# Kernel optimization log

Hardware: AMD Instinct MI355X
Metric: run time of the kernel (lower is better)

The kernel has to match this reference:

```python
import jax, jax.numpy as jnp
import numpy as np

N, C, T, F = 32, 64, 256, 64  # batch, EEG channels, time samples, freq bands


def setup_inputs() -> dict:
    key = jax.random.key(0)
    X = jax.random.normal(key, (N, C, T, F), dtype=jnp.float32)
    gammad = jnp.zeros((), dtype=jnp.float32)  # learned scalar, init 'zeros'
    return {"X": X, "gammad": gammad}


def reference(X, gammad):
    # X: (N, C, T, F) -> (N, F, C, T)
    Xp = jnp.transpose(X, (0, 3, 1, 2))
    # squared norms per channel: (N, F, C, 1)
    R = jnp.sum(Xp * Xp, axis=-1, keepdims=True)
    # Gram matrix over time axis: (N, F, C, C)
    G = jnp.einsum('nfct,nfkt->nfck', Xp, Xp)
    # pairwise squared Euclidean distances between channels
    D = R - 2.0 * G + jnp.swapaxes(R, -1, -2)
    # strictly-upper-triangular entries (excludes diagonal), per (n, f)
    iu, ju = jnp.triu_indices(D.shape[-1], k=1)
    triu = jnp.sqrt(D[..., iu, ju])  # (N, F, C*(C-1)/2)
    # median bandwidth (tfp.stats.percentile q=50 uses 'nearest' interpolation)
    sigma = jnp.quantile(triu, 0.5, axis=-1, method='nearest')  # (N, F)
    denom = 2.0 * jnp.power(10.0, gammad) * jnp.square(sigma)   # (N, F)
    A = jnp.exp(-D / denom[..., None, None])  # (N, F, C, C) RBF affinity
    return A
```

## Files before the change

kernel.cpp:

```cpp
#include <hip/hip_runtime.h>
#include <stdint.h>

typedef _Float16 f16x8 __attribute__((ext_vector_type(8)));
typedef float f32x4 __attribute__((ext_vector_type(4)));

__device__ __forceinline__ uint32_t pack2(float a, float b) {
    union { _Float16 h[2]; uint32_t u; } p;
    p.h[0] = (_Float16)a; p.h[1] = (_Float16)b;
    return p.u;
}

__device__ __forceinline__ uint16_t key16(float v) {
    _Float16 hx = (_Float16)fmaxf(v, 0.0f);
    return __builtin_bit_cast(uint16_t, hx);
}

__device__ __forceinline__ f32x4 MF(f16x8 a, f16x8 b, f32x4 c) {
    return __builtin_amdgcn_mfma_f32_16x16x32_f16(a, b, c, 0, 0, 0);
}

__global__ __launch_bounds__(512, 2)
void gfc_main(const float* __restrict__ X, const float* __restrict__ gp,
              float* __restrict__ out) {
    __shared__ __align__(16) unsigned char XS[65536];
    __shared__ float Rbuf[4][64];

    int j = blockIdx.x;
    int xcd = j & 7, s = j >> 3;
    int gi = s >> 2, fq4 = s & 3;
    int g = gi * 8 + xcd;
    int n = g >> 2, f16g = g & 3;
    int f0 = f16g * 16 + fq4 * 4;

    int tid = threadIdx.x;
    int wid = tid >> 6, lane = tid & 63;
    int w4 = wid & 3, hi = wid >> 2;
    int l4 = lane & 15, lg = lane >> 4;

    float p10 = exp2f(gp[0] * 3.3219280948873623f);
    const float* Xn = X + (size_t)n * 1048576 + f0;

    f32x4 dd[2][4];
    #pragma unroll
    for (int a = 0; a < 2; ++a)
        #pragma unroll
        for (int b = 0; b < 4; ++b) dd[a][b] = f32x4{0, 0, 0, 0};

    float4 pv[8][2];

    auto load_chunk = [&](int t0) {
        #pragma unroll
        for (int k = 0; k < 8; ++k) {
            int c = k * 8 + wid;
            const float* p = Xn + (size_t)c * 16384 + t0 * 64 + lane * 128;
            pv[k][0] = *(const float4*)p;
            pv[k][1] = *(const float4*)(p + 64);
        }
    };
    auto write_chunk = [&]() {
        #pragma unroll
        for (int k = 0; k < 8; ++k) {
            int c = k * 8 + wid;
            int o = c * 256 + ((lane * 4) ^ ((c & 7) << 4));
            *(uint32_t*)(XS + o)         = pack2(pv[k][0].x, pv[k][1].x);
            *(uint32_t*)(XS + 16384 + o) = pack2(pv[k][0].y, pv[k][1].y);
            *(uint32_t*)(XS + 32768 + o) = pack2(pv[k][0].z, pv[k][1].z);
            *(uint32_t*)(XS + 49152 + o) = pack2(pv[k][0].w, pv[k][1].w);
        }
    };
    auto gram_buf = [&]() {
        const unsigned char* bp = XS + w4 * 16384;
        #pragma unroll
        for (int ks = 0; ks < 4; ++ks) {
            f16x8 fr[4];
            #pragma unroll
            for (int i2 = 0; i2 < 4; ++i2)
                fr[i2] = *(const f16x8*)(bp + (i2 * 16 + l4) * 256 +
                                         ((ks * 64 + lg * 16) ^ ((l4 & 7) << 4)));
            if (!hi) {
                #pragma unroll
                for (int tj = 0; tj < 4; ++tj) {
                    dd[0][tj] = MF(fr[tj], fr[0], dd[0][tj]);
                    dd[1][tj] = MF(fr[tj], fr[1], dd[1][tj]);
                }
            } else {
                #pragma unroll
                for (int tj = 0; tj < 4; ++tj) {
                    dd[0][tj] = MF(fr[tj], fr[2], dd[0][tj]);
                    dd[1][tj] = MF(fr[tj], fr[3], dd[1][tj]);
                }
            }
        }
    };

    load_chunk(0);
    write_chunk();
    load_chunk(128);
    __syncthreads();

    gram_buf();
    __syncthreads();

    write_chunk();
    __syncthreads();

    gram_buf();

    {
        f32x4 dg0 = hi ? dd[0][2] : dd[0][0];
        f32x4 dg1 = hi ? dd[1][3] : dd[1][1];
        if (lg == (l4 >> 2)) {
            int r = l4 & 3;
            float v0 = r == 0 ? dg0[0] : r == 1 ? dg0[1] : r == 2 ? dg0[2] : dg0[3];
            float v1 = r == 0 ? dg1[0] : r == 1 ? dg1[1] : r == 2 ? dg1[2] : dg1[3];
            Rbuf[w4][(hi * 2) * 16 + l4] = v0;
            Rbuf[w4][(hi * 2 + 1) * 16 + l4] = v1;
        }
    }
    __syncthreads();

    float Rr0 = Rbuf[w4][(hi * 2) * 16 + l4];
    float Rr1 = Rbuf[w4][(hi * 2 + 1) * 16 + l4];
    #pragma unroll
    for (int tj = 0; tj < 4; ++tj) {
        f32x4 Rc = *(const f32x4*)&Rbuf[w4][tj * 16 + lg * 4];
        #pragma unroll
        for (int r = 0; r < 4; ++r) {
            dd[0][tj][r] = Rr0 + Rc[r] - 2.0f * dd[0][tj][r];
            dd[1][tj][r] = Rr1 + Rc[r] - 2.0f * dd[1][tj][r];
        }
    }

    uint32_t pk[32];
    #pragma unroll
    for (int tt = 0; tt < 2; ++tt) {
        int row = (hi * 2 + tt) * 16 + l4;
        #pragma unroll
        for (int tj = 0; tj < 4; ++tj)
            #pragma unroll
            for (int rp = 0; rp < 2; ++rp) {
                int col0 = tj * 16 + lg * 4 + 2 * rp;
                uint32_t k0 = (row < col0)     ? key16(dd[tt][tj][2 * rp])     : 0x7FFFu;
                uint32_t k1 = (row < col0 + 1) ? key16(dd[tt][tj][2 * rp + 1]) : 0x7FFFu;
                pk[tt * 8 + tj * 2 + rp] = k0 | (k1 << 16);
            }
    }

    {
        uint32_t* base = (uint32_t*)(XS + w4 * 16384);
        uint32_t* mywr = base + hi * 1024;
        #pragma unroll
        for (int e = 0; e < 16; ++e) mywr[e * 64 + lane] = pk[e];
        __syncthreads();
        const uint32_t* prd = base + (hi ^ 1) * 1024;
        #pragma unroll
        for (int e = 0; e < 16; ++e) pk[16 + e] = prd[e * 64 + lane];
    }

    int u = 0;
    for (int bit = 14; bit >= 0; --bit) {
        uint32_t cand = (uint32_t)(u | (1 << bit));
        int cnt = 0;
        #pragma unroll
        for (int i = 0; i < 32; ++i) {
            cnt += ((pk[i] & 0xFFFFu) < cand) ? 1 : 0;
            cnt += ((pk[i] >> 16) < cand) ? 1 : 0;
        }
        #pragma unroll
        for (int off = 32; off; off >>= 1) cnt += __shfl_xor(cnt, off, 64);
        if (cnt <= 1008) u |= (1 << bit);
    }
    float sigma2 = (float)__builtin_bit_cast(_Float16, (uint16_t)u);
    float ninv = -1.0f / (2.0f * p10 * sigma2);

    float* op = out + ((size_t)(n * 64 + f0 + w4) << 12);
    #pragma unroll
    for (int tt = 0; tt < 2; ++tt) {
        int row = (hi * 2 + tt) * 16 + l4;
        #pragma unroll
        for (int tj = 0; tj < 4; ++tj) {
            float4 rv;
            rv.x = __expf(dd[tt][tj][0] * ninv);
            rv.y = __expf(dd[tt][tj][1] * ninv);
            rv.z = __expf(dd[tt][tj][2] * ninv);
            rv.w = __expf(dd[tt][tj][3] * ninv);
            *(float4*)(op + row * 64 + tj * 16 + lg * 4) = rv;
        }
    }
}

extern "C" void kernel_launch(void* const* d_in, const int* in_sizes, int n_in,
                              void* d_out, int out_size, void* d_ws, size_t ws_size,
                              hipStream_t stream) {
    (void)in_sizes; (void)n_in; (void)out_size; (void)d_ws; (void)ws_size;
    const float* X  = (const float*)d_in[0];
    const float* gp = (const float*)d_in[1];
    float* out = (float*)d_out;
    gfc_main<<<512, 512, 0, stream>>>(X, gp, out);
}
```

Baseline: 78.32 us.

## Add fp16 transpose prepass into workspace and read it directly in Gram kernel

A new prep kernel reads X with coalesced loads, converts it to fp16 and transposes it through shared memory into a workspace laid out as (n, f, c, t). The main kernel then loads MFMA fragments straight from that workspace, with no LDS staging and no strided fp32 gathers. This targets the poorly coalesced 16-byte strided reads of the original single kernel. The cost is a second launch plus an extra 64 MB write and read through the workspace. The old kernel is kept as a fallback when the workspace is too small.

```diff
diff --git a/kernel.cpp b/kernel.cpp
--- a/kernel.cpp
+++ b/kernel.cpp
@@ -4,10 +4,13 @@
 typedef _Float16 f16x8 __attribute__((ext_vector_type(8)));
 typedef float f32x4 __attribute__((ext_vector_type(4)));
 
-__device__ __forceinline__ uint32_t pack2(float a, float b) {
-    union { _Float16 h[2]; uint32_t u; } p;
-    p.h[0] = (_Float16)a; p.h[1] = (_Float16)b;
-    return p.u;
+__device__ __forceinline__ f32x4 MF(f16x8 a, f16x8 b, f32x4 c) {
+    return __builtin_amdgcn_mfma_f32_16x16x32_f16(a, b, c, 0, 0, 0);
+}
+
+__device__ __forceinline__ uint16_t h16(float v) {
+    _Float16 h = (_Float16)v;
+    return __builtin_bit_cast(uint16_t, h);
 }
 
 __device__ __forceinline__ uint16_t key16(float v) {
@@ -15,39 +18,206 @@
     return __builtin_bit_cast(uint16_t, hx);
 }
 
-__device__ __forceinline__ f32x4 MF(f16x8 a, f16x8 b, f32x4 c) {
-    return __builtin_amdgcn_mfma_f32_16x16x32_f16(a, b, c, 0, 0, 0);
+__device__ __forceinline__ uint32_t pack2(float a, float b) {
+    return (uint32_t)h16(a) | ((uint32_t)h16(b) << 16);
+}
+
+__global__ __launch_bounds__(256)
+void gfc_prep(const float* __restrict__ X, uint16_t* __restrict__ W) {
+    __shared__ uint16_t T[256 * 66];
+    int n = blockIdx.x >> 6, c = blockIdx.x & 63;
+    int tid = threadIdx.x;
+    const float* src = X + ((size_t)n * 64 + c) * 16384;
+
+    #pragma unroll
+    for (int rb = 0; rb < 2; ++rb) {
+        float4 v[8];
+        #pragma unroll
+        for (int i = 0; i < 8; ++i) {
+            int o = (rb * 8 + i) * 256 + tid;
+            v[i] = *(const float4*)(src + (size_t)o * 4);
+        }
+        #pragma unroll
+        for (int i = 0; i < 8; ++i) {
+            int o = (rb * 8 + i) * 256 + tid;
+            int t = o >> 4, fj = o & 15;
+            uint16_t* row = &T[t * 66 + fj * 4];
+            row[0] = h16(v[i].x);
+            row[1] = h16(v[i].y);
+            row[2] = h16(v[i].z);
+            row[3] = h16(v[i].w);
+        }
+    }
+    __syncthreads();
+
+    int f = tid >> 2, q = tid & 3;
+    uint16_t* dst = W + (((size_t)n * 64 + f) * 64 + c) * 256 + q * 64;
+    #pragma unroll
+    for (int jj = 0; jj < 8; ++jj) {
+        uint32_t w[4];
+        #pragma unroll
+        for (int p = 0; p < 4; ++p) {
+            int t = q * 64 + jj * 8 + p * 2;
+            uint32_t lo = T[t * 66 + f];
+            uint32_t hi = T[(t + 1) * 66 + f];
+            w[p] = lo | (hi << 16);
+        }
+        *(uint4*)(dst + jj * 8) = *(uint4*)w;
+    }
 }
 
 __global__ __launch_bounds__(512, 2)
-void gfc_main(const float* __restrict__ X, const float* __restrict__ gp,
-              float* __restrict__ out) {
+void gfc_main2(const uint16_t* __restrict__ W, const float* __restrict__ gp,
+               float* __restrict__ out) {
+    __shared__ float Rbuf[4][64];
+    __shared__ uint32_t EX[8][1024];
+
+    int j = blockIdx.x;
+    int xcd = j & 7, r = j >> 3;
+    int fq = r & 15, nh = r >> 4;
+    int n = xcd * 4 + nh;
+    int f0 = fq * 4;
+
+    int tid = threadIdx.x;
+    int wid = tid >> 6, lane = tid & 63;
+    int w4 = wid & 3, hi = wid >> 2;
+    int l4 = lane & 15, lg = lane >> 4;
+
+    float p10 = exp2f(gp[0] * 3.3219280948873623f);
+    const uint16_t* Wf = W + ((size_t)n * 64 + f0 + w4) * 16384;
+
+    f32x4 dd[2][4];
+    #pragma unroll
+    for (int a = 0; a < 2; ++a)
+        #pragma unroll
+        for (int b = 0; b < 4; ++b) dd[a][b] = f32x4{0, 0, 0, 0};
+
+    #pragma unroll
+    for (int ks = 0; ks < 8; ++ks) {
+        f16x8 fr[4];
+        #pragma unroll
+        for (int i2 = 0; i2 < 4; ++i2)
+            fr[i2] = *(const f16x8*)(Wf + (i2 * 16 + l4) * 256 + ks * 32 + lg * 8);
+        if (!hi) {
+            #pragma unroll
+            for (int tj = 0; tj < 4; ++tj) {
+                dd[0][tj] = MF(fr[tj], fr[0], dd[0][tj]);
+                dd[1][tj] = MF(fr[tj], fr[1], dd[1][tj]);
+            }
+        } else {
+            #pragma unroll
+            for (int tj = 0; tj < 4; ++tj) {
+                dd[0][tj] = MF(fr[tj], fr[2], dd[0][tj]);
+                dd[1][tj] = MF(fr[tj], fr[3], dd[1][tj]);
+            }
+        }
+    }
+
+    {
+        f32x4 dg0 = hi ? dd[0][2] : dd[0][0];
+        f32x4 dg1 = hi ? dd[1][3] : dd[1][1];
+        if (lg == (l4 >> 2)) {
+            int rr = l4 & 3;
+            float v0 = rr == 0 ? dg0[0] : rr == 1 ? dg0[1] : rr == 2 ? dg0[2] : dg0[3];
+            float v1 = rr == 0 ? dg1[0] : rr == 1 ? dg1[1] : rr == 2 ? dg1[2] : dg1[3];
+            Rbuf[w4][(hi * 2) * 16 + l4] = v0;
+            Rbuf[w4][(hi * 2 + 1) * 16 + l4] = v1;
+        }
+    }
+    __syncthreads();
+
+    float Rr0 = Rbuf[w4][(hi * 2) * 16 + l4];
+    float Rr1 = Rbuf[w4][(hi * 2 + 1) * 16 + l4];
+    #pragma unroll
+    for (int tj = 0; tj < 4; ++tj) {
+        f32x4 Rc = *(const f32x4*)&Rbuf[w4][tj * 16 + lg * 4];
+        #pragma unroll
+        for (int rr = 0; rr < 4; ++rr) {
+            dd[0][tj][rr] = Rr0 + Rc[rr] - 2.0f * dd[0][tj][rr];
+            dd[1][tj][rr] = Rr1 + Rc[rr] - 2.0f * dd[1][tj][rr];
+        }
+    }
+
+    uint32_t pk[32];
+    #pragma unroll
+    for (int tt = 0; tt < 2; ++tt) {
+        int row = (hi * 2 + tt) * 16 + l4;
+        #pragma unroll
+        for (int tj = 0; tj < 4; ++tj)
+            #pragma unroll
+            for (int rp = 0; rp < 2; ++rp) {
+                int col0 = tj * 16 + lg * 4 + 2 * rp;
+                uint32_t k0 = (row < col0)     ? key16(dd[tt][tj][2 * rp])     : 0x7FFFu;
+                uint32_t k1 = (row < col0 + 1) ? key16(dd[tt][tj][2 * rp + 1]) : 0x7FFFu;
+                pk[tt * 8 + tj * 2 + rp] = k0 | (k1 << 16);
+            }
+    }
+
+    {
+        uint32_t* mywr = EX[wid];
+        #pragma unroll
+        for (int e = 0; e < 16; ++e) mywr[e * 64 + lane] = pk[e];
+        __syncthreads();
+        const uint32_t* prd = EX[wid ^ 4];
+        #pragma unroll
+        for (int e = 0; e < 16; ++e) pk[16 + e] = prd[e * 64 + lane];
+    }
+
+    int u = 0;
+    for (int bit = 14; bit >= 0; --bit) {
+        uint32_t cand = (uint32_t)(u | (1 << bit));
+        int cnt = 0;
+        #pragma unroll
+        for (int i = 0; i < 32; ++i) {
+            cnt += ((pk[i] & 0xFFFFu) < cand) ? 1 : 0;
+            cnt += ((pk[i] >> 16) < cand) ? 1 : 0;
+        }
+        #pragma unroll
+        for (int off = 32; off; off >>= 1) cnt += __shfl_xor(cnt, off, 64);
+        if (cnt <= 1008) u |= (1 << bit);
+    }
+    float sigma2 = (float)__builtin_bit_cast(_Float16, (uint16_t)u);
+    float ninv = -1.0f / (2.0f * p10 * sigma2);
+
+    float* op = out + ((size_t)(n * 64 + f0 + w4) << 12);
+    #pragma unroll
+    for (int tt = 0; tt < 2; ++tt) {
+        int row = (hi * 2 + tt) * 16 + l4;
+        #pragma unroll
+        for (int tj = 0; tj < 4; ++tj) {
+            float4 rv;
+            rv.x = __expf(dd[tt][tj][0] * ninv);
+            rv.y = __expf(dd[tt][tj][1] * ninv);
+            rv.z = __expf(dd[tt][tj][2] * ninv);
+            rv.w = __expf(dd[tt][tj][3] * ninv);
+            *(float4*)(op + row * 64 + tj * 16 + lg * 4) = rv;
+        }
+    }
+}
+
+__global__ __launch_bounds__(512, 2)
+void gfc_fb(const float* __restrict__ X, const float* __restrict__ gp,
+            float* __restrict__ out) {
     __shared__ __align__(16) unsigned char XS[65536];
     __shared__ float Rbuf[4][64];
-
     int j = blockIdx.x;
     int xcd = j & 7, s = j >> 3;
     int gi = s >> 2, fq4 = s & 3;
     int g = gi * 8 + xcd;
     int n = g >> 2, f16g = g & 3;
     int f0 = f16g * 16 + fq4 * 4;
-
     int tid = threadIdx.x;
     int wid = tid >> 6, lane = tid & 63;
     int w4 = wid & 3, hi = wid >> 2;
     int l4 = lane & 15, lg = lane >> 4;
-
     float p10 = exp2f(gp[0] * 3.3219280948873623f);
     const float* Xn = X + (size_t)n * 1048576 + f0;
-
     f32x4 dd[2][4];
     #pragma unroll
     for (int a = 0; a < 2; ++a)
         #pragma unroll
         for (int b = 0; b < 4; ++b) dd[a][b] = f32x4{0, 0, 0, 0};
-
     float4 pv[8][2];
-
     auto load_chunk = [&](int t0) {
         #pragma unroll
         for (int k = 0; k < 8; ++k) {
@@ -92,45 +262,38 @@
             }
         }
     };
-
     load_chunk(0);
     write_chunk();
     load_chunk(128);
     __syncthreads();
-
     gram_buf();
     __syncthreads();
-
     write_chunk();
     __syncthreads();
-
     gram_buf();
-
     {
         f32x4 dg0 = hi ? dd[0][2] : dd[0][0];
         f32x4 dg1 = hi ? dd[1][3] : dd[1][1];
         if (lg == (l4 >> 2)) {
-            int r = l4 & 3;
-            float v0 = r == 0 ? dg0[0] : r == 1 ? dg0[1] : r == 2 ? dg0[2] : dg0[3];
-            float v1 = r == 0 ? dg1[0] : r == 1 ? dg1[1] : r == 2 ? dg1[2] : dg1[3];
+            int rr = l4 & 3;
+            float v0 = rr == 0 ? dg0[0] : rr == 1 ? dg0[1] : rr == 2 ? dg0[2] : dg0[3];
+            float v1 = rr == 0 ? dg1[0] : rr == 1 ? dg1[1] : rr == 2 ? dg1[2] : dg1[3];
             Rbuf[w4][(hi * 2) * 16 + l4] = v0;
             Rbuf[w4][(hi * 2 + 1) * 16 + l4] = v1;
         }
     }
     __syncthreads();
-
     float Rr0 = Rbuf[w4][(hi * 2) * 16 + l4];
     float Rr1 = Rbuf[w4][(hi * 2 + 1) * 16 + l4];
     #pragma unroll
     for (int tj = 0; tj < 4; ++tj) {
         f32x4 Rc = *(const f32x4*)&Rbuf[w4][tj * 16 + lg * 4];
         #pragma unroll
-        for (int r = 0; r < 4; ++r) {
-            dd[0][tj][r] = Rr0 + Rc[r] - 2.0f * dd[0][tj][r];
-            dd[1][tj][r] = Rr1 + Rc[r] - 2.0f * dd[1][tj][r];
-        }
-    }
-
+        for (int rr = 0; rr < 4; ++rr) {
+            dd[0][tj][rr] = Rr0 + Rc[rr] - 2.0f * dd[0][tj][rr];
+            dd[1][tj][rr] = Rr1 + Rc[rr] - 2.0f * dd[1][tj][rr];
+        }
+    }
     uint32_t pk[32];
     #pragma unroll
     for (int tt = 0; tt < 2; ++tt) {
@@ -145,7 +308,6 @@
                 pk[tt * 8 + tj * 2 + rp] = k0 | (k1 << 16);
             }
     }
-
     {
         uint32_t* base = (uint32_t*)(XS + w4 * 16384);
         uint32_t* mywr = base + hi * 1024;
@@ -156,7 +318,6 @@
         #pragma unroll
         for (int e = 0; e < 16; ++e) pk[16 + e] = prd[e * 64 + lane];
     }
-
     int u = 0;
     for (int bit = 14; bit >= 0; --bit) {
         uint32_t cand = (uint32_t)(u | (1 << bit));
@@ -172,7 +333,6 @@
     }
     float sigma2 = (float)__builtin_bit_cast(_Float16, (uint16_t)u);
     float ninv = -1.0f / (2.0f * p10 * sigma2);
-
     float* op = out + ((size_t)(n * 64 + f0 + w4) << 12);
     #pragma unroll
     for (int tt = 0; tt < 2; ++tt) {
@@ -192,9 +352,15 @@
 extern "C" void kernel_launch(void* const* d_in, const int* in_sizes, int n_in,
                               void* d_out, int out_size, void* d_ws, size_t ws_size,
                               hipStream_t stream) {
-    (void)in_sizes; (void)n_in; (void)out_size; (void)d_ws; (void)ws_size;
+    (void)in_sizes; (void)n_in; (void)out_size;
     const float* X  = (const float*)d_in[0];
     const float* gp = (const float*)d_in[1];
-    float* out = (float*)d_out;
-    gfc_main<<<512, 512, 0, stream>>>(X, gp, out);
-}
+    float* outp = (float*)d_out;
+    if (ws_size >= (size_t)67108864) {
+        uint16_t* W = (uint16_t*)d_ws;
+        gfc_prep<<<2048, 256, 0, stream>>>(X, W);
+        gfc_main2<<<512, 512, 0, stream>>>(W, gp, outp);
+    } else {
+        gfc_fb<<<512, 512, 0, stream>>>(X, gp, outp);
+    }
+}
```

New measurement: 76.56 us. -2.3%, faster.

## Stage input via direct global-to-LDS loads with double-buffered 8-step pipeline

Applied to the files above, without the earlier changes.

Replaces the register-staged load/convert/write of two 128-sample chunks with eight 32-sample chunks. Each chunk is copied as raw fp32 directly into LDS with global_load_lds, falling back to plain loads, using an XOR swizzle and two alternating 32KB buffers. Conversion to fp16 now happens when MFMA fragments are read from LDS. The goal is to overlap global loads with the Gram MFMAs and cut register pressure and VGPR round-trips. In exchange there are more barriers, scalar 4-byte LDS reads per fragment, and conversion work repeated inside the compute loop.

```diff
diff --git a/kernel.cpp b/kernel.cpp
--- a/kernel.cpp
+++ b/kernel.cpp
@@ -4,10 +4,8 @@
 typedef _Float16 f16x8 __attribute__((ext_vector_type(8)));
 typedef float f32x4 __attribute__((ext_vector_type(4)));
 
-__device__ __forceinline__ uint32_t pack2(float a, float b) {
-    union { _Float16 h[2]; uint32_t u; } p;
-    p.h[0] = (_Float16)a; p.h[1] = (_Float16)b;
-    return p.u;
+__device__ __forceinline__ f32x4 MF(f16x8 a, f16x8 b, f32x4 c) {
+    return __builtin_amdgcn_mfma_f32_16x16x32_f16(a, b, c, 0, 0, 0);
 }
 
 __device__ __forceinline__ uint16_t key16(float v) {
@@ -15,9 +13,14 @@
     return __builtin_bit_cast(uint16_t, hx);
 }
 
-__device__ __forceinline__ f32x4 MF(f16x8 a, f16x8 b, f32x4 c) {
-    return __builtin_amdgcn_mfma_f32_16x16x32_f16(a, b, c, 0, 0, 0);
-}
+#if defined(__has_builtin)
+# if __has_builtin(__builtin_amdgcn_global_load_lds)
+#  define HAVE_GLDS 1
+# endif
+#endif
+#ifndef HAVE_GLDS
+# define HAVE_GLDS 0
+#endif
 
 __global__ __launch_bounds__(512, 2)
 void gfc_main(const float* __restrict__ X, const float* __restrict__ gp,
@@ -36,9 +39,10 @@
     int wid = tid >> 6, lane = tid & 63;
     int w4 = wid & 3, hi = wid >> 2;
     int l4 = lane & 15, lg = lane >> 4;
+    int pos = lane & 31, cs = lane >> 5;
 
     float p10 = exp2f(gp[0] * 3.3219280948873623f);
-    const float* Xn = X + (size_t)n * 1048576 + f0;
+    const unsigned char* Xb = (const unsigned char*)(X + (size_t)n * 1048576 + f0);
 
     f32x4 dd[2][4];
     #pragma unroll
@@ -46,65 +50,66 @@
         #pragma unroll
         for (int b = 0; b < 4; ++b) dd[a][b] = f32x4{0, 0, 0, 0};
 
-    float4 pv[8][2];
-
-    auto load_chunk = [&](int t0) {
-        #pragma unroll
-        for (int k = 0; k < 8; ++k) {
-            int c = k * 8 + wid;
-            const float* p = Xn + (size_t)c * 16384 + t0 * 64 + lane * 128;
-            pv[k][0] = *(const float4*)p;
-            pv[k][1] = *(const float4*)(p + 64);
+    auto stage = [&](int bsel, int T0) {
+        unsigned char* bb = XS + bsel * 32768;
+        #pragma unroll
+        for (int i = 0; i < 4; ++i) {
+            int c0 = wid * 8 + i * 2;
+            int c  = c0 + cs;
+            int tt = pos ^ (c & 15);
+            const unsigned char* gsrc = Xb + (size_t)c * 65536 + (size_t)(T0 + tt) * 256;
+#if HAVE_GLDS
+            __builtin_amdgcn_global_load_lds(
+                (const uint32_t __attribute__((address_space(1)))*)(uintptr_t)gsrc,
+                (uint32_t __attribute__((address_space(3)))*)(uintptr_t)(bb + c0 * 512),
+                16, 0, 0);
+#else
+            *(uint4*)(bb + c0 * 512 + lane * 16) = *(const uint4*)gsrc;
+#endif
         }
     };
-    auto write_chunk = [&]() {
-        #pragma unroll
-        for (int k = 0; k < 8; ++k) {
-            int c = k * 8 + wid;
-            int o = c * 256 + ((lane * 4) ^ ((c & 7) << 4));
-            *(uint32_t*)(XS + o)         = pack2(pv[k][0].x, pv[k][1].x);
-            *(uint32_t*)(XS + 16384 + o) = pack2(pv[k][0].y, pv[k][1].y);
-            *(uint32_t*)(XS + 32768 + o) = pack2(pv[k][0].z, pv[k][1].z);
-            *(uint32_t*)(XS + 49152 + o) = pack2(pv[k][0].w, pv[k][1].w);
+
+    auto gram = [&](int bsel) {
+        const float* B = (const float*)(XS + bsel * 32768);
+        f16x8 fr[4];
+        #pragma unroll
+        for (int i2 = 0; i2 < 4; ++i2) {
+            int c = i2 * 16 + l4;
+            int base = c * 128 + w4;
+            float v[8];
+            #pragma unroll
+            for (int jj = 0; jj < 8; ++jj) {
+                int tl = lg * 8 + jj;
+                v[jj] = B[base + (((tl ^ l4)) << 2)];
+            }
+            f16x8 f;
+            #pragma unroll
+            for (int jj = 0; jj < 8; ++jj) f[jj] = (_Float16)v[jj];
+            fr[i2] = f;
+        }
+        if (!hi) {
+            #pragma unroll
+            for (int tj = 0; tj < 4; ++tj) {
+                dd[0][tj] = MF(fr[tj], fr[0], dd[0][tj]);
+                dd[1][tj] = MF(fr[tj], fr[1], dd[1][tj]);
+            }
+        } else {
+            #pragma unroll
+            for (int tj = 0; tj < 4; ++tj) {
+                dd[0][tj] = MF(fr[tj], fr[2], dd[0][tj]);
+                dd[1][tj] = MF(fr[tj], fr[3], dd[1][tj]);
+            }
         }
     };
-    auto gram_buf = [&]() {
-        const unsigned char* bp = XS + w4 * 16384;
-        #pragma unroll
-        for (int ks = 0; ks < 4; ++ks) {
-            f16x8 fr[4];
-            #pragma unroll
-            for (int i2 = 0; i2 < 4; ++i2)
-                fr[i2] = *(const f16x8*)(bp + (i2 * 16 + l4) * 256 +
-                                         ((ks * 64 + lg * 16) ^ ((l4 & 7) << 4)));
-            if (!hi) {
-                #pragma unroll
-                for (int tj = 0; tj < 4; ++tj) {
-                    dd[0][tj] = MF(fr[tj], fr[0], dd[0][tj]);
-                    dd[1][tj] = MF(fr[tj], fr[1], dd[1][tj]);
-                }
-            } else {
-                #pragma unroll
-                for (int tj = 0; tj < 4; ++tj) {
-                    dd[0][tj] = MF(fr[tj], fr[2], dd[0][tj]);
-                    dd[1][tj] = MF(fr[tj], fr[3], dd[1][tj]);
-                }
-            }
-        }
-    };
-
-    load_chunk(0);
-    write_chunk();
-    load_chunk(128);
+
+    stage(0, 0);
     __syncthreads();
-
-    gram_buf();
-    __syncthreads();
-
-    write_chunk();
-    __syncthreads();
-
-    gram_buf();
+    #pragma unroll
+    for (int k = 0; k < 8; ++k) {
+        if (k < 7) stage((k + 1) & 1, (k + 1) * 32);
+        gram(k & 1);
+        if (k < 7) __syncthreads();
+    }
 
     {
         f32x4 dg0 = hi ? dd[0][2] : dd[0][0];
@@ -147,7 +152,7 @@
     }
 
     {
-        uint32_t* base = (uint32_t*)(XS + w4 * 16384);
+        uint32_t* base = (uint32_t*)(XS + w4 * 8192);
         uint32_t* mywr = base + hi * 1024;
         #pragma unroll
         for (int e = 0; e < 16; ++e) mywr[e * 64 + lane] = pk[e];
```

Result: faster. 67.89 us (-13.3%).

## Halve LDS footprint with four 64-step time chunks to raise occupancy

Applied to the files above, without the earlier changes.

The time axis is now processed in four 64-sample chunks through a 32KB shared buffer instead of two 128-sample chunks through 64KB, and launch bounds ask for four blocks per CU instead of two. The per-thread load mapping also changes so that all 512 threads share the chunk loads, with fewer registers held per thread. The aim is more resident waves to hide global-load latency, at the cost of twice as many barriers and no prefetch of the next chunk overlapping the MFMA work. With only 512 blocks, the extra occupancy may go partly unused.

```diff
diff --git a/kernel.cpp b/kernel.cpp
--- a/kernel.cpp
+++ b/kernel.cpp
@@ -4,25 +4,23 @@
 typedef _Float16 f16x8 __attribute__((ext_vector_type(8)));
 typedef float f32x4 __attribute__((ext_vector_type(4)));
 
+__device__ __forceinline__ uint16_t h16(float v) {
+    _Float16 h = (_Float16)v; return __builtin_bit_cast(uint16_t, h);
+}
+__device__ __forceinline__ uint16_t key16(float v) {
+    _Float16 h = (_Float16)fmaxf(v, 0.0f); return __builtin_bit_cast(uint16_t, h);
+}
 __device__ __forceinline__ uint32_t pack2(float a, float b) {
-    union { _Float16 h[2]; uint32_t u; } p;
-    p.h[0] = (_Float16)a; p.h[1] = (_Float16)b;
-    return p.u;
+    return (uint32_t)h16(a) | ((uint32_t)h16(b) << 16);
 }
-
-__device__ __forceinline__ uint16_t key16(float v) {
-    _Float16 hx = (_Float16)fmaxf(v, 0.0f);
-    return __builtin_bit_cast(uint16_t, hx);
-}
-
 __device__ __forceinline__ f32x4 MF(f16x8 a, f16x8 b, f32x4 c) {
     return __builtin_amdgcn_mfma_f32_16x16x32_f16(a, b, c, 0, 0, 0);
 }
 
-__global__ __launch_bounds__(512, 2)
+__global__ __launch_bounds__(512, 4)
 void gfc_main(const float* __restrict__ X, const float* __restrict__ gp,
               float* __restrict__ out) {
-    __shared__ __align__(16) unsigned char XS[65536];
+    __shared__ __align__(16) unsigned char XS[32768];
     __shared__ float Rbuf[4][64];
 
     int j = blockIdx.x;
@@ -46,36 +44,35 @@
         #pragma unroll
         for (int b = 0; b < 4; ++b) dd[a][b] = f32x4{0, 0, 0, 0};
 
-    float4 pv[8][2];
+    for (int ch = 0; ch < 4; ++ch) {
+        float4 va[4], vb[4];
+        #pragma unroll
+        for (int it = 0; it < 4; ++it) {
+            int item = it * 512 + tid;
+            int c = item >> 5, tp = item & 31;
+            const float* p = Xn + ((size_t)c * 256 + ch * 64 + 2 * tp) * 64;
+            va[it] = *(const float4*)p;
+            vb[it] = *(const float4*)(p + 64);
+        }
+        #pragma unroll
+        for (int it = 0; it < 4; ++it) {
+            int item = it * 512 + tid;
+            int c = item >> 5, tp = item & 31;
+            int o = c * 128 + ((tp * 4) ^ ((c & 7) << 4));
+            *(uint32_t*)(XS + o)         = pack2(va[it].x, vb[it].x);
+            *(uint32_t*)(XS +  8192 + o) = pack2(va[it].y, vb[it].y);
+            *(uint32_t*)(XS + 16384 + o) = pack2(va[it].z, vb[it].z);
+            *(uint32_t*)(XS + 24576 + o) = pack2(va[it].w, vb[it].w);
+        }
+        __syncthreads();
 
-    auto load_chunk = [&](int t0) {
+        const unsigned char* bp = XS + w4 * 8192;
         #pragma unroll
-        for (int k = 0; k < 8; ++k) {
-            int c = k * 8 + wid;
-            const float* p = Xn + (size_t)c * 16384 + t0 * 64 + lane * 128;
-            pv[k][0] = *(const float4*)p;
-            pv[k][1] = *(const float4*)(p + 64);
-        }
-    };
-    auto write_chunk = [&]() {
-        #pragma unroll
-        for (int k = 0; k < 8; ++k) {
-            int c = k * 8 + wid;
-            int o = c * 256 + ((lane * 4) ^ ((c & 7) << 4));
-            *(uint32_t*)(XS + o)         = pack2(pv[k][0].x, pv[k][1].x);
-            *(uint32_t*)(XS + 16384 + o) = pack2(pv[k][0].y, pv[k][1].y);
-            *(uint32_t*)(XS + 32768 + o) = pack2(pv[k][0].z, pv[k][1].z);
-            *(uint32_t*)(XS + 49152 + o) = pack2(pv[k][0].w, pv[k][1].w);
-        }
-    };
-    auto gram_buf = [&]() {
-        const unsigned char* bp = XS + w4 * 16384;
-        #pragma unroll
-        for (int ks = 0; ks < 4; ++ks) {
+        for (int ks = 0; ks < 2; ++ks) {
             f16x8 fr[4];
             #pragma unroll
             for (int i2 = 0; i2 < 4; ++i2)
-                fr[i2] = *(const f16x8*)(bp + (i2 * 16 + l4) * 256 +
+                fr[i2] = *(const f16x8*)(bp + (i2 * 16 + l4) * 128 +
                                          ((ks * 64 + lg * 16) ^ ((l4 & 7) << 4)));
             if (!hi) {
                 #pragma unroll
@@ -91,20 +88,8 @@
                 }
             }
         }
-    };
-
-    load_chunk(0);
-    write_chunk();
-    load_chunk(128);
-    __syncthreads();
-
-    gram_buf();
-    __syncthreads();
-
-    write_chunk();
-    __syncthreads();
-
-    gram_buf();
+        __syncthreads();
+    }
 
     {
         f32x4 dg0 = hi ? dd[0][2] : dd[0][0];
@@ -147,12 +132,11 @@
     }
 
     {
-        uint32_t* base = (uint32_t*)(XS + w4 * 16384);
-        uint32_t* mywr = base + hi * 1024;
+        uint32_t* mywr = (uint32_t*)(XS + wid * 4096);
         #pragma unroll
         for (int e = 0; e < 16; ++e) mywr[e * 64 + lane] = pk[e];
         __syncthreads();
-        const uint32_t* prd = base + (hi ^ 1) * 1024;
+        const uint32_t* prd = (const uint32_t*)(XS + (wid ^ 4) * 4096);
         #pragma unroll
         for (int e = 0; e < 16; ++e) pk[16 + e] = prd[e * 64 + lane];
     }
```

New measurement: 69.26 us. 11.6% less time.
